# Performance work log

Hardware: AMD Instinct MI355X
Metric: run time of the kernel (lower is better)

## Reference

```python
import jax, jax.numpy as jnp
import numpy as np

EMBED = 768
HEADS = 12
DEPTH = 12
FEAT = 2048


def _ln(x, w, b, eps=1e-6):
    m = x.mean(-1, keepdims=True)
    v = ((x - m) ** 2).mean(-1, keepdims=True)
    return (x - m) * jax.lax.rsqrt(v + eps) * w + b


def _var_attn(x, mbias, Wqkv, bqkv, Wp, bp, h, f):
    # x: (B, N, D) with N = 1 + f*n ; mbias: (B, N) additive mask (0 or -100)
    B, N, D = x.shape
    d = D // h
    n = (N - 1) // f
    scale = d ** -0.5
    qkv = x @ Wqkv.T + bqkv
    q, k, v = jnp.split(qkv, 3, axis=-1)
    hd = lambda t: t.reshape(B, N, h, d).transpose(0, 2, 1, 3)  # (B,h,N,d)
    q = hd(q) * scale
    k = hd(k)
    v = hd(v)
    # cls token attends to everything
    cls_sim = jnp.einsum('bhd,bhjd->bhj', q[:, :, 0], k) + mbias[:, None, :]
    cls_out = jnp.einsum('bhj,bhjd->bhd', jax.nn.softmax(cls_sim, axis=-1), v)[:, :, None, :]
    # spatial tokens attend within their frame plus the cls token
    q_ = q[:, :, 1:].reshape(B, h, f, n, d)
    k_ = jnp.concatenate([jnp.broadcast_to(k[:, :, None, 0:1, :], (B, h, f, 1, d)),
                          k[:, :, 1:].reshape(B, h, f, n, d)], axis=3)
    v_ = jnp.concatenate([jnp.broadcast_to(v[:, :, None, 0:1, :], (B, h, f, 1, d)),
                          v[:, :, 1:].reshape(B, h, f, n, d)], axis=3)
    mcat = jnp.concatenate([jnp.broadcast_to(mbias[:, 0][:, None, None], (B, f, 1)),
                            mbias[:, 1:].reshape(B, f, n)], axis=2)  # (B,f,n+1)
    sim = jnp.einsum('bhfid,bhfjd->bhfij', q_, k_) + mcat[:, None, :, None, :]
    out = jnp.einsum('bhfij,bhfjd->bhfid', jax.nn.softmax(sim, axis=-1), v_)
    out = out.reshape(B, h, f * n, d)
    out = jnp.concatenate([cls_out, out], axis=2).transpose(0, 2, 1, 3).reshape(B, N, D)
    return out @ Wp.T + bp


def setup_inputs() -> dict:
    key = jax.random.key(0)
    ks = jax.random.split(key, 12)
    B, F, L = 256, 4, 20
    std = 0.02
    p = {}
    p['x'] = jax.random.normal(ks[0], (B, F, L, 2054), dtype=jnp.float32)
    p['x_mask'] = jax.random.randint(ks[1], (B, F, L), 0, 2, dtype=jnp.int32)
    p['obj_W'] = (jax.random.normal(ks[2], (EMBED, FEAT)) * std).astype(jnp.float32)
    p['obj_b'] = jnp.zeros((EMBED,), jnp.float32)
    p['pos_W'] = (jax.random.normal(ks[3], (EMBED, 6)) * std).astype(jnp.float32)
    p['pos_b'] = jnp.zeros((EMBED,), jnp.float32)
    p['cls_token'] = (jax.random.normal(ks[4], (1, 1, EMBED)) * std).astype(jnp.float32)
    p['cls_pos'] = (jax.random.normal(ks[5], (1, L + 1, EMBED)) * std).astype(jnp.float32)
    p['temporal_embed'] = jnp.zeros((1, F, EMBED), jnp.float32)
    p['ln1_w'] = jnp.ones((DEPTH, EMBED), jnp.float32)
    p['ln1_b'] = jnp.zeros((DEPTH, EMBED), jnp.float32)
    p['ln2_w'] = jnp.ones((DEPTH, EMBED), jnp.float32)
    p['ln2_b'] = jnp.zeros((DEPTH, EMBED), jnp.float32)
    p['qkv_W'] = (jax.random.normal(ks[6], (DEPTH, 3 * EMBED, EMBED)) * std).astype(jnp.float32)
    p['qkv_b'] = jnp.zeros((DEPTH, 3 * EMBED), jnp.float32)
    p['ap_W'] = (jax.random.normal(ks[7], (DEPTH, EMBED, EMBED)) * std).astype(jnp.float32)
    p['ap_b'] = jnp.zeros((DEPTH, EMBED), jnp.float32)
    p['fc1_W'] = (jax.random.normal(ks[8], (DEPTH, 4 * EMBED, EMBED)) * std).astype(jnp.float32)
    p['fc1_b'] = jnp.zeros((DEPTH, 4 * EMBED), jnp.float32)
    p['fc2_W'] = (jax.random.normal(ks[9], (DEPTH, EMBED, 4 * EMBED)) * std).astype(jnp.float32)
    p['fc2_b'] = jnp.zeros((DEPTH, EMBED), jnp.float32)
    p['proj_W'] = (jax.random.normal(ks[10], (256, EMBED)) * std).astype(jnp.float32)
    return p


def reference(x, x_mask, obj_W, obj_b, pos_W, pos_b, cls_token, cls_pos, temporal_embed,
              ln1_w, ln1_b, ln2_w, ln2_b, qkv_W, qkv_b, ap_W, ap_b,
              fc1_W, fc1_b, fc2_W, fc2_b, proj_W):
    B, F, L, _ = x.shape
    tok = x[..., :FEAT] @ obj_W.T + obj_b + (x[..., FEAT:] @ pos_W.T + pos_b)
    tok = tok.reshape(B, F * L, EMBED)
    m = x_mask.reshape(B, F * L).astype(tok.dtype)
    tok = jnp.concatenate([jnp.broadcast_to(cls_token, (B, 1, EMBED)), tok], axis=1)
    m = jnp.concatenate([jnp.ones((B, 1), tok.dtype), m], axis=1)
    mbias = (m - 1.0) * 100.0  # 0 for valid, -100 for padded
    pos_total = jnp.concatenate([cls_pos[:, 0:1, :], jnp.repeat(temporal_embed, L, axis=1)], axis=1)
    tok = tok + pos_total

    def body(xc, p):
        l1w, l1b, qW, qb, aW, ab, l2w, l2b, f1W, f1b, f2W, f2b = p
        a = _var_attn(_ln(xc, l1w, l1b), mbias, qW, qb, aW, ab, HEADS, F)
        xr = xc + a
        xc = xr + (jax.nn.gelu(_ln(xr, l2w, l2b) @ f1W.T + f1b, approximate=False) @ f2W.T + f2b)
        return xc, None

    tok, _ = jax.lax.scan(body, tok, (ln1_w, ln1_b, qkv_W, qkv_b, ap_W, ap_b,
                                      ln2_w, ln2_b, fc1_W, fc1_b, fc2_W, fc2_b))
    return tok @ proj_W.T, mbias
```

## Files before the change

kernel.cpp:

```cpp
#include <hip/hip_runtime.h>

typedef __bf16 bf16;
typedef __bf16 bf16x8 __attribute__((ext_vector_type(8)));
typedef float f32x4 __attribute__((ext_vector_type(4)));

#define EMBED 768
#define HEADS 12
#define DEPTH 12
#define B_ 256
#define F_ 4
#define L_ 20
#define NTOK 81
#define ROWS (B_ * NTOK)
#define SROWS (B_ * F_ * L_)

#define GLOAD16(g, l)                                                              \
    __builtin_amdgcn_global_load_lds((const __attribute__((address_space(1))) void*)(g), \
                                     (__attribute__((address_space(3))) void*)(l), 16, 0, 0)

__device__ __forceinline__ float fast_gelu(float v) {
    float x = v * 0.70710678118654752f;
    float ax = fabsf(x);
    float t = __fdividef(1.f, fmaf(0.3275911f, ax, 1.f));
    float p = ((((1.061405429f * t - 1.453152027f) * t + 1.421413741f) * t -
                0.284496736f) * t + 0.254829592f) * t;
    float e = __expf(-ax * ax);
    float erfv = copysignf(1.f - p * e, x);
    return 0.5f * v * (1.f + erfv);
}

__global__ __launch_bounds__(256) void repack_kernel(const float* __restrict__ x,
                                                     bf16* __restrict__ xr) {
    int row = blockIdx.x;
    const float* src = x + (size_t)row * 2054;
    bf16* dst = xr + (size_t)row * 2048;
    int t = threadIdx.x;
    int e0 = t * 8;
    bf16 tmp[8];
#pragma unroll
    for (int i = 0; i < 4; ++i) {
        float2 v = *(const float2*)&src[e0 + 2 * i];
        tmp[2 * i] = (bf16)v.x;
        tmp[2 * i + 1] = (bf16)v.y;
    }
    *(uint4*)&dst[e0] = *(const uint4*)tmp;
}

__global__ __launch_bounds__(256) void w2bf_kernel(const float* __restrict__ src,
                                                   bf16* __restrict__ dst) {
    size_t i = ((size_t)blockIdx.x * 256 + threadIdx.x) * 8;
    float4 a = *(const float4*)&src[i];
    float4 b = *(const float4*)&src[i + 4];
    bf16 t[8] = {(bf16)a.x, (bf16)a.y, (bf16)a.z, (bf16)a.w,
                 (bf16)b.x, (bf16)b.y, (bf16)b.z, (bf16)b.w};
    *(uint4*)&dst[i] = *(const uint4*)t;
}

template <int FUSE, bool ROWMAP, typename CT>
__global__ __launch_bounds__(256) void gemm_bb(const bf16* __restrict__ A, int lda,
                                               const bf16* __restrict__ W,
                                               const float* __restrict__ bias,
                                               const bf16* __restrict__ R,
                                               CT* __restrict__ C, int N, int K) {
    __shared__ __align__(16) bf16 As[128 * 64];
    __shared__ __align__(16) bf16 Ws[128 * 64];

    const int tid = threadIdx.x;
    const int lane = tid & 63;
    const int wv = tid >> 6;
    const int wm = (wv & 1) * 64;
    const int wn = (wv >> 1) * 64;
    const int lr = lane & 15;
    const int lq = lane >> 4;

    const int GX = gridDim.x;
    const int nwg = GX * gridDim.y;
    const int flat = blockIdx.y * GX + blockIdx.x;
    const int xcd = flat & 7, pos = flat >> 3;
    const int qc = nwg >> 3, rc = nwg & 7;
    const int wg = (xcd < rc ? xcd * (qc + 1) : rc * (qc + 1) + (xcd - rc) * qc) + pos;
    const int n0 = (wg % GX) * 128;
    const int m0 = (wg / GX) * 128;

    const int srow = lane >> 3;
    const int scol = 8 * ((lane & 7) ^ srow);
    const bf16* aB = A + (size_t)(m0 + srow) * lda + scol;
    const bf16* wB = W + (size_t)(n0 + srow) * K + scol;

    f32x4 acc[4][4];
#pragma unroll
    for (int i = 0; i < 4; ++i)
#pragma unroll
        for (int j = 0; j < 4; ++j) acc[i][j] = (f32x4){0.f, 0.f, 0.f, 0.f};

    const int swz = (lr & 7) << 4;

    for (int k0 = 0; k0 < K; k0 += 64) {
#pragma unroll
        for (int i = 0; i < 4; ++i) {
            const int ch = wv * 4 + i;
            GLOAD16(aB + (size_t)(ch * 8) * lda + k0, &As[ch * 512]);
            GLOAD16(wB + (size_t)(ch * 8) * K + k0, &Ws[ch * 512]);
        }
        __syncthreads();
#pragma unroll
        for (int kk = 0; kk < 2; ++kk) {
            const int co = (((kk << 6) | (lq << 4)) ^ swz) >> 1;
            bf16x8 af[4], bw[4];
#pragma unroll
            for (int t = 0; t < 4; ++t) {
                af[t] = *(const bf16x8*)&As[(wm + t * 16 + lr) * 64 + co];
                bw[t] = *(const bf16x8*)&Ws[(wn + t * 16 + lr) * 64 + co];
            }
#pragma unroll
            for (int mi = 0; mi < 4; ++mi)
#pragma unroll
                for (int ni = 0; ni < 4; ++ni)
                    acc[mi][ni] = __builtin_amdgcn_mfma_f32_16x16x32_bf16(af[mi], bw[ni],
                                                                          acc[mi][ni], 0, 0, 0);
        }
        __syncthreads();
    }

#pragma unroll
    for (int mi = 0; mi < 4; ++mi) {
#pragma unroll
        for (int ni = 0; ni < 4; ++ni) {
            int gcol = n0 + wn + ni * 16 + lr;
            float bv = bias ? bias[gcol] : 0.f;
#pragma unroll
            for (int r = 0; r < 4; ++r) {
                int grow = m0 + wm + mi * 16 + lq * 4 + r;
                float v = acc[mi][ni][r] + bv;
                if (FUSE == 1) v = fast_gelu(v);
                if (FUSE == 2) v += (float)R[(size_t)grow * N + gcol];
                int orow = grow;
                if (ROWMAP) orow = grow + grow / 80 + 1;
                C[(size_t)orow * N + gcol] = (CT)v;
            }
        }
    }
}

template <int FUSE, bool ROWMAP, typename CT>
__global__ __launch_bounds__(256) void gemm_bt(const bf16* __restrict__ A, int lda,
                                               const float* __restrict__ W,
                                               const float* __restrict__ bias,
                                               const bf16* __restrict__ R,
                                               CT* __restrict__ C, int N, int K) {
    __shared__ __align__(16) bf16 As[128][32];
    __shared__ __align__(16) bf16 Ws[128][32];

    const int tid = threadIdx.x;
    const int lane = tid & 63;
    const int wv = tid >> 6;
    const int wm = (wv & 1) * 64;
    const int wn = (wv >> 1) * 64;
    const int lr = lane & 15;
    const int lq = lane >> 4;
    const int m0 = blockIdx.x * 128;
    const int n0 = blockIdx.y * 128;

    f32x4 acc[4][4];
#pragma unroll
    for (int i = 0; i < 4; ++i)
#pragma unroll
        for (int j = 0; j < 4; ++j) acc[i][j] = (f32x4){0.f, 0.f, 0.f, 0.f};

    for (int k0 = 0; k0 < K; k0 += 32) {
#pragma unroll
        for (int i = 0; i < 2; ++i) {
            int c = tid + 256 * i;
            int row = c >> 2;
            int kc = (c & 3) * 8;
            *(uint4*)&As[row][kc] = *(const uint4*)&A[(size_t)(m0 + row) * lda + k0 + kc];
        }
#pragma unroll
        for (int i = 0; i < 4; ++i) {
            int c = tid + 256 * i;
            int row = c >> 3;
            int kc = (c & 7) * 4;
            float4 v = *(const float4*)&W[(size_t)(n0 + row) * K + k0 + kc];
            bf16 wb[4] = {(bf16)v.x, (bf16)v.y, (bf16)v.z, (bf16)v.w};
            *(uint2*)&Ws[row][kc] = *(const uint2*)wb;
        }
        __syncthreads();
        bf16x8 af[4], bf_[4];
#pragma unroll
        for (int t = 0; t < 4; ++t) {
            af[t] = *(const bf16x8*)&As[wm + t * 16 + lr][lq * 8];
            bf_[t] = *(const bf16x8*)&Ws[wn + t * 16 + lr][lq * 8];
        }
#pragma unroll
        for (int mi = 0; mi < 4; ++mi)
#pragma unroll
            for (int ni = 0; ni < 4; ++ni)
                acc[mi][ni] = __builtin_amdgcn_mfma_f32_16x16x32_bf16(af[mi], bf_[ni],
                                                                      acc[mi][ni], 0, 0, 0);
        __syncthreads();
    }

#pragma unroll
    for (int mi = 0; mi < 4; ++mi) {
#pragma unroll
        for (int ni = 0; ni < 4; ++ni) {
            int gcol = n0 + wn + ni * 16 + lr;
            float bv = bias ? bias[gcol] : 0.f;
#pragma unroll
            for (int r = 0; r < 4; ++r) {
                int grow = m0 + wm + mi * 16 + lq * 4 + r;
                float v = acc[mi][ni][r] + bv;
                if (FUSE == 1) v = fast_gelu(v);
                if (FUSE == 2) v += (float)R[(size_t)grow * N + gcol];
                int orow = grow;
                if (ROWMAP) orow = grow + grow / 80 + 1;
                C[(size_t)orow * N + gcol] = (CT)v;
            }
        }
    }
}

__global__ __launch_bounds__(256) void embed_finish(const float* __restrict__ x,
                                                    const float* __restrict__ posW,
                                                    const float* __restrict__ posb,
                                                    const float* __restrict__ temb,
                                                    bf16* __restrict__ tok) {
    int r = blockIdx.x;
    int fr = (r % 80) / 20;
    int orow = r + r / 80 + 1;
    __shared__ float pf[6];
    if (threadIdx.x < 6) pf[threadIdx.x] = x[(size_t)r * 2054 + 2048 + threadIdx.x];
    __syncthreads();
    int t = threadIdx.x;
#pragma unroll
    for (int i = 0; i < 3; ++i) {
        int c = t + 256 * i;
        float v = posb[c] + temb[fr * EMBED + c];
#pragma unroll
        for (int j = 0; j < 6; ++j) v += pf[j] * posW[c * 6 + j];
        size_t idx = (size_t)orow * EMBED + c;
        tok[idx] = (bf16)((float)tok[idx] + v);
    }
}

__global__ __launch_bounds__(256) void cls_mbias_kernel(const float* __restrict__ cls_tok,
                                                        const float* __restrict__ cls_pos,
                                                        const int* __restrict__ xmask,
                                                        bf16* __restrict__ tok,
                                                        float* __restrict__ mbias,
                                                        float* __restrict__ out1) {
    int b = blockIdx.x;
    int t = threadIdx.x;
#pragma unroll
    for (int i = 0; i < 3; ++i) {
        int c = t + 256 * i;
        tok[(size_t)(b * NTOK) * EMBED + c] = (bf16)(cls_tok[c] + cls_pos[c]);
    }
    if (t < NTOK) {
        float mv = (t == 0) ? 0.f : ((float)xmask[b * 80 + t - 1] - 1.f) * 100.f;
        mbias[b * NTOK + t] = mv;
        out1[b * NTOK + t] = mv;
    }
}

__global__ __launch_bounds__(256) void ln_kernel(const bf16* __restrict__ X,
                                                 const float* __restrict__ w,
                                                 const float* __restrict__ b,
                                                 bf16* __restrict__ Y) {
    int row = blockIdx.x;
    int t = threadIdx.x;
    float xv[8];
    float s = 0.f, ss = 0.f;
    if (t < 96) {
        bf16x8 v8 = *(const bf16x8*)&X[(size_t)row * EMBED + t * 8];
#pragma unroll
        for (int i = 0; i < 8; ++i) {
            float v = (float)v8[i];
            xv[i] = v;
            s += v;
            ss += v * v;
        }
    }
#pragma unroll
    for (int off = 32; off; off >>= 1) {
        s += __shfl_down(s, off);
        ss += __shfl_down(ss, off);
    }
    __shared__ float ws_s[4], ws_q[4];
    int wv = t >> 6, lane = t & 63;
    if (lane == 0) { ws_s[wv] = s; ws_q[wv] = ss; }
    __syncthreads();
    s = ws_s[0] + ws_s[1];
    ss = ws_q[0] + ws_q[1];
    float mean = s * (1.f / 768.f);
    float var = ss * (1.f / 768.f) - mean * mean;
    float inv = rsqrtf(fmaxf(var, 0.f) + 1e-6f);
    if (t < 96) {
        float4 w0 = *(const float4*)&w[t * 8];
        float4 w1 = *(const float4*)&w[t * 8 + 4];
        float4 b0 = *(const float4*)&b[t * 8];
        float4 b1 = *(const float4*)&b[t * 8 + 4];
        float wr[8] = {w0.x, w0.y, w0.z, w0.w, w1.x, w1.y, w1.z, w1.w};
        float br[8] = {b0.x, b0.y, b0.z, b0.w, b1.x, b1.y, b1.z, b1.w};
        bf16 ob[8];
#pragma unroll
        for (int i = 0; i < 8; ++i) ob[i] = (bf16)((xv[i] - mean) * inv * wr[i] + br[i]);
        *(uint4*)&Y[(size_t)row * EMBED + t * 8] = *(const uint4*)ob;
    }
}

__global__ __launch_bounds__(256) void attn_kernel(const bf16* __restrict__ qkv,
                                                   const float* __restrict__ mbias,
                                                   bf16* __restrict__ aout) {
    int bh = blockIdx.x;
    int b = bh / HEADS, h = bh % HEADS;
    __shared__ __align__(16) float Qf[NTOK][68];
    __shared__ __align__(16) float Kf[NTOK][68];
    __shared__ __align__(16) bf16 Vs[NTOK][72];
    __shared__ float S[80][22];
    __shared__ float Sc[96];
    __shared__ float MB[NTOK];
    const size_t base = (size_t)(b * NTOK) * 2304 + h * 64;
    int t = threadIdx.x;

    for (int ch = t; ch < NTOK * 8; ch += 256) {
        int r = ch >> 3, c8 = (ch & 7) * 8;
        size_t o = base + (size_t)r * 2304 + c8;
        bf16x8 qv = *(const bf16x8*)&qkv[o];
        bf16x8 kv = *(const bf16x8*)&qkv[o + 768];
        *(uint4*)&Vs[r][c8] = *(const uint4*)&qkv[o + 1536];
        float4 q0 = {(float)qv[0], (float)qv[1], (float)qv[2], (float)qv[3]};
        float4 q1 = {(float)qv[4], (float)qv[5], (float)qv[6], (float)qv[7]};
        float4 k0 = {(float)kv[0], (float)kv[1], (float)kv[2], (float)kv[3]};
        float4 k1 = {(float)kv[4], (float)kv[5], (float)kv[6], (float)kv[7]};
        *(float4*)&Qf[r][c8] = q0;
        *(float4*)&Qf[r][c8 + 4] = q1;
        *(float4*)&Kf[r][c8] = k0;
        *(float4*)&Kf[r][c8 + 4] = k1;
    }
    if (t < NTOK) MB[t] = mbias[b * NTOK + t];
    __syncthreads();

    {
        int qt, kst, kstep, klim;
        if (t < 240) {
            int qi = t / 3;
            qt = 1 + qi;
            kst = t - qi * 3;
            kstep = 3;
            klim = 21;
        } else {
            qt = 0;
            kst = t - 240;
            kstep = 16;
            klim = NTOK;
        }
        float fq[64];
#pragma unroll
        for (int i = 0; i < 16; ++i) {
            float4 v = *(const float4*)&Qf[qt][i * 4];
            fq[4 * i] = v.x; fq[4 * i + 1] = v.y; fq[4 * i + 2] = v.z; fq[4 * i + 3] = v.w;
        }
        if (t < 240) {
            int qi = t / 3, fb = (qi / 20) * 20;
            for (int kj = kst; kj < klim; kj += kstep) {
                int kt = (kj == 0) ? 0 : fb + kj;
                float acc = 0.f;
#pragma unroll
                for (int i = 0; i < 16; ++i) {
                    float4 kv = *(const float4*)&Kf[kt][i * 4];
                    acc += fq[4 * i] * kv.x + fq[4 * i + 1] * kv.y +
                           fq[4 * i + 2] * kv.z + fq[4 * i + 3] * kv.w;
                }
                S[qi][kj] = acc * 0.125f + MB[kt];
            }
        } else {
            for (int kt = kst; kt < klim; kt += kstep) {
                float acc = 0.f;
#pragma unroll
                for (int i = 0; i < 16; ++i) {
                    float4 kv = *(const float4*)&Kf[kt][i * 4];
                    acc += fq[4 * i] * kv.x + fq[4 * i + 1] * kv.y +
                           fq[4 * i + 2] * kv.z + fq[4 * i + 3] * kv.w;
                }
                Sc[kt] = acc * 0.125f + MB[kt];
            }
        }
    }
    __syncthreads();

    if (t < 80) {
        float mx = -1e30f;
        for (int j = 0; j < 21; ++j) mx = fmaxf(mx, S[t][j]);
        float sum = 0.f;
        for (int j = 0; j < 21; ++j) { float e = __expf(S[t][j] - mx); S[t][j] = e; sum += e; }
        float rs = 1.f / sum;
        for (int j = 0; j < 21; ++j) S[t][j] *= rs;
    } else if (t == 80) {
        float mx = -1e30f;
        for (int j = 0; j < NTOK; ++j) mx = fmaxf(mx, Sc[j]);
        float sum = 0.f;
        for (int j = 0; j < NTOK; ++j) { float e = __expf(Sc[j] - mx); Sc[j] = e; sum += e; }
        float rs = 1.f / sum;
        for (int j = 0; j < NTOK; ++j) Sc[j] *= rs;
    }
    __syncthreads();

    for (int idx = t; idx < NTOK * 8; idx += 256) {
        int r = idx >> 3, c8 = (idx & 7) * 8;
        float acc[8];
#pragma unroll
        for (int q = 0; q < 8; ++q) acc[q] = 0.f;
        if (r == 0) {
            for (int j = 0; j < NTOK; ++j) {
                float w = Sc[j];
                bf16x8 vv = *(const bf16x8*)&Vs[j][c8];
#pragma unroll
                for (int q = 0; q < 8; ++q) acc[q] += w * (float)vv[q];
            }
        } else {
            int qi = r - 1, fb = (qi / 20) * 20;
            {
                float w = S[qi][0];
                bf16x8 vv = *(const bf16x8*)&Vs[0][c8];
#pragma unroll
                for (int q = 0; q < 8; ++q) acc[q] += w * (float)vv[q];
            }
            for (int j = 1; j < 21; ++j) {
                float w = S[qi][j];
                bf16x8 vv = *(const bf16x8*)&Vs[fb + j][c8];
#pragma unroll
                for (int q = 0; q < 8; ++q) acc[q] += w * (float)vv[q];
            }
        }
        bf16 ob[8];
#pragma unroll
        for (int q = 0; q < 8; ++q) ob[q] = (bf16)acc[q];
        *(uint4*)&aout[(size_t)(b * NTOK + r) * EMBED + h * 64 + c8] = *(const uint4*)ob;
    }
}

extern "C" void kernel_launch(void* const* d_in, const int* in_sizes, int n_in,
                              void* d_out, int out_size, void* d_ws, size_t ws_size,
                              hipStream_t stream) {
    const float* x = (const float*)d_in[0];
    const int* xmask = (const int*)d_in[1];
    const float* objW = (const float*)d_in[2];
    const float* objb = (const float*)d_in[3];
    const float* posW = (const float*)d_in[4];
    const float* posb = (const float*)d_in[5];
    const float* clsT = (const float*)d_in[6];
    const float* clsP = (const float*)d_in[7];
    const float* temb = (const float*)d_in[8];
    const float* ln1w = (const float*)d_in[9];
    const float* ln1b = (const float*)d_in[10];
    const float* ln2w = (const float*)d_in[11];
    const float* ln2b = (const float*)d_in[12];
    const float* qkvW = (const float*)d_in[13];
    const float* qkvb = (const float*)d_in[14];
    const float* apW = (const float*)d_in[15];
    const float* apb = (const float*)d_in[16];
    const float* f1W = (const float*)d_in[17];
    const float* f1b = (const float*)d_in[18];
    const float* f2W = (const float*)d_in[19];
    const float* f2b = (const float*)d_in[20];
    const float* projW = (const float*)d_in[21];

    char* ws = (char*)d_ws;
    bf16* tok = (bf16*)(ws);
    bf16* s1 = (bf16*)(ws + (size_t)(32 << 20));
    float* mb = (float*)(ws + (size_t)(64 << 20));
    bf16* big = (bf16*)(ws + (size_t)(65 << 20));
    float* out0 = (float*)d_out;
    float* out1 = out0 + (size_t)ROWS * 256;

    const size_t WOFF = (size_t)192 << 20;
    const size_t E_OBJ = (size_t)768 * 2048;
    const size_t E_QKV = (size_t)DEPTH * 2304 * 768;
    const size_t E_AP = (size_t)DEPTH * 768 * 768;
    const size_t E_FC = (size_t)DEPTH * 3072 * 768;
    const size_t E_PROJ = (size_t)256 * 768;
    const size_t WTOT = (E_OBJ + E_QKV + E_AP + 2 * E_FC + E_PROJ) * 2;
    const bool bigws = ws_size >= WOFF + WTOT;

    if (bigws) {
        bf16* objW16 = (bf16*)(ws + WOFF);
        bf16* qkvW16 = objW16 + E_OBJ;
        bf16* apW16 = qkvW16 + E_QKV;
        bf16* fc1W16 = apW16 + E_AP;
        bf16* fc2W16 = fc1W16 + E_FC;
        bf16* projW16 = fc2W16 + E_FC;

        w2bf_kernel<<<(int)(E_OBJ / 2048), 256, 0, stream>>>(objW, objW16);
        w2bf_kernel<<<(int)(E_QKV / 2048), 256, 0, stream>>>(qkvW, qkvW16);
        w2bf_kernel<<<(int)(E_AP / 2048), 256, 0, stream>>>(apW, apW16);
        w2bf_kernel<<<(int)(E_FC / 2048), 256, 0, stream>>>(f1W, fc1W16);
        w2bf_kernel<<<(int)(E_FC / 2048), 256, 0, stream>>>(f2W, fc2W16);
        w2bf_kernel<<<(int)(E_PROJ / 2048), 256, 0, stream>>>(projW, projW16);

        repack_kernel<<<SROWS, 256, 0, stream>>>(x, big);
        gemm_bb<0, true, bf16><<<dim3(EMBED / 128, SROWS / 128), 256, 0, stream>>>(
            big, 2048, objW16, objb, nullptr, tok, EMBED, 2048);
        embed_finish<<<SROWS, 256, 0, stream>>>(x, posW, posb, temb, tok);
        cls_mbias_kernel<<<B_, 256, 0, stream>>>(clsT, clsP, xmask, tok, mb, out1);

        for (int l = 0; l < DEPTH; ++l) {
            ln_kernel<<<ROWS, 256, 0, stream>>>(tok, ln1w + l * EMBED, ln1b + l * EMBED, s1);
            gemm_bb<0, false, bf16><<<dim3(2304 / 128, ROWS / 128), 256, 0, stream>>>(
                s1, EMBED, qkvW16 + (size_t)l * 2304 * 768, qkvb + l * 2304, nullptr, big,
                2304, EMBED);
            attn_kernel<<<B_ * HEADS, 256, 0, stream>>>(big, mb, s1);
            gemm_bb<2, false, bf16><<<dim3(EMBED / 128, ROWS / 128), 256, 0, stream>>>(
                s1, EMBED, apW16 + (size_t)l * 768 * 768, apb + l * EMBED, tok, tok, EMBED,
                EMBED);
            ln_kernel<<<ROWS, 256, 0, stream>>>(tok, ln2w + l * EMBED, ln2b + l * EMBED, s1);
            gemm_bb<1, false, bf16><<<dim3(3072 / 128, ROWS / 128), 256, 0, stream>>>(
                s1, EMBED, fc1W16 + (size_t)l * 3072 * 768, f1b + l * 3072, nullptr, big,
                3072, EMBED);
            gemm_bb<2, false, bf16><<<dim3(EMBED / 128, ROWS / 128), 256, 0, stream>>>(
                big, 3072, fc2W16 + (size_t)l * 3072 * 768, f2b + l * EMBED, tok, tok, EMBED,
                3072);
        }

        gemm_bb<0, false, float><<<dim3(256 / 128, ROWS / 128), 256, 0, stream>>>(
            tok, EMBED, projW16, nullptr, nullptr, out0, 256, EMBED);
    } else {
        repack_kernel<<<SROWS, 256, 0, stream>>>(x, big);
        gemm_bt<0, true, bf16><<<dim3(SROWS / 128, EMBED / 128), 256, 0, stream>>>(
            big, 2048, objW, objb, nullptr, tok, EMBED, 2048);
        embed_finish<<<SROWS, 256, 0, stream>>>(x, posW, posb, temb, tok);
        cls_mbias_kernel<<<B_, 256, 0, stream>>>(clsT, clsP, xmask, tok, mb, out1);

        for (int l = 0; l < DEPTH; ++l) {
            ln_kernel<<<ROWS, 256, 0, stream>>>(tok, ln1w + l * EMBED, ln1b + l * EMBED, s1);
            gemm_bt<0, false, bf16><<<dim3(ROWS / 128, 2304 / 128), 256, 0, stream>>>(
                s1, EMBED, qkvW + (size_t)l * 2304 * EMBED, qkvb + l * 2304, nullptr, big,
                2304, EMBED);
            attn_kernel<<<B_ * HEADS, 256, 0, stream>>>(big, mb, s1);
            gemm_bt<2, false, bf16><<<dim3(ROWS / 128, EMBED / 128), 256, 0, stream>>>(
                s1, EMBED, apW + (size_t)l * EMBED * EMBED, apb + l * EMBED, tok, tok, EMBED,
                EMBED);
            ln_kernel<<<ROWS, 256, 0, stream>>>(tok, ln2w + l * EMBED, ln2b + l * EMBED, s1);
            gemm_bt<1, false, bf16><<<dim3(ROWS / 128, 3072 / 128), 256, 0, stream>>>(
                s1, EMBED, f1W + (size_t)l * 3072 * EMBED, f1b + l * 3072, nullptr, big, 3072,
                EMBED);
            gemm_bt<2, false, bf16><<<dim3(ROWS / 128, EMBED / 128), 256, 0, stream>>>(
                big, 3072, f2W + (size_t)l * EMBED * 3072, f2b + l * EMBED, tok, tok, EMBED,
                3072);
        }

        gemm_bt<0, false, float><<<dim3(ROWS / 128, 256 / 128), 256, 0, stream>>>(
            tok, EMBED, projW, nullptr, nullptr, out0, 256, EMBED);
    }
}
```

Baseline: 7.552 ms.

## Stage GEMM epilogue through LDS for vectorized stores; pack two rows per LN block

The bf16 GEMM epilogue now writes each 16-row accumulator tile into a per-wave LDS patch, then reads it back so each lane handles 8 contiguous columns. This allows 16-byte vector loads of the residual and vector stores of the output, replacing scattered 2-byte accesses. LayerNorm now processes two rows per 256-thread block instead of one, so fewer threads sit idle and half as many blocks are launched. The attention score loop was also cleaned up by simplifying its index setup. The staging adds LDS round trips in the epilogue.

```diff
diff --git a/kernel.cpp b/kernel.cpp
--- a/kernel.cpp
+++ b/kernel.cpp
@@ -62,8 +62,7 @@
                                                const float* __restrict__ bias,
                                                const bf16* __restrict__ R,
                                                CT* __restrict__ C, int N, int K) {
-    __shared__ __align__(16) bf16 As[128 * 64];
-    __shared__ __align__(16) bf16 Ws[128 * 64];
+    __shared__ __align__(16) char smem[32768];
 
     const int tid = threadIdx.x;
     const int lane = tid & 63;
@@ -87,6 +86,9 @@
     const bf16* aB = A + (size_t)(m0 + srow) * lda + scol;
     const bf16* wB = W + (size_t)(n0 + srow) * K + scol;
 
+    bf16* As = (bf16*)smem;
+    bf16* Ws = (bf16*)(smem + 16384);
+
     f32x4 acc[4][4];
 #pragma unroll
     for (int i = 0; i < 4; ++i)
@@ -99,8 +101,8 @@
 #pragma unroll
         for (int i = 0; i < 4; ++i) {
             const int ch = wv * 4 + i;
-            GLOAD16(aB + (size_t)(ch * 8) * lda + k0, &As[ch * 512]);
-            GLOAD16(wB + (size_t)(ch * 8) * K + k0, &Ws[ch * 512]);
+            GLOAD16(aB + (size_t)(ch * 8) * lda + k0, smem + ch * 1024);
+            GLOAD16(wB + (size_t)(ch * 8) * K + k0, smem + 16384 + ch * 1024);
         }
         __syncthreads();
 #pragma unroll
@@ -122,21 +124,46 @@
         __syncthreads();
     }
 
+    float* patch = (float*)(smem + wv * 4352);
+    float bv4[4];
+#pragma unroll
+    for (int ni = 0; ni < 4; ++ni) bv4[ni] = bias ? bias[n0 + wn + ni * 16 + lr] : 0.f;
+    const int rr = lane >> 3;
+    const int c8 = (lane & 7) * 8;
 #pragma unroll
     for (int mi = 0; mi < 4; ++mi) {
 #pragma unroll
-        for (int ni = 0; ni < 4; ++ni) {
-            int gcol = n0 + wn + ni * 16 + lr;
-            float bv = bias ? bias[gcol] : 0.f;
-#pragma unroll
-            for (int r = 0; r < 4; ++r) {
-                int grow = m0 + wm + mi * 16 + lq * 4 + r;
-                float v = acc[mi][ni][r] + bv;
-                if (FUSE == 1) v = fast_gelu(v);
-                if (FUSE == 2) v += (float)R[(size_t)grow * N + gcol];
-                int orow = grow;
-                if (ROWMAP) orow = grow + grow / 80 + 1;
-                C[(size_t)orow * N + gcol] = (CT)v;
+        for (int ni = 0; ni < 4; ++ni)
+#pragma unroll
+            for (int r = 0; r < 4; ++r)
+                patch[(lq * 4 + r) * 68 + ni * 16 + lr] = acc[mi][ni][r] + bv4[ni];
+#pragma unroll
+        for (int hf = 0; hf < 2; ++hf) {
+            int row = rr + hf * 8;
+            float v[8];
+            *(float4*)&v[0] = *(const float4*)&patch[row * 68 + c8];
+            *(float4*)&v[4] = *(const float4*)&patch[row * 68 + c8 + 4];
+            int grow = m0 + wm + mi * 16 + row;
+            int gcol = n0 + wn + c8;
+            if (FUSE == 1) {
+#pragma unroll
+                for (int q = 0; q < 8; ++q) v[q] = fast_gelu(v[q]);
+            }
+            if (FUSE == 2) {
+                bf16x8 rv = *(const bf16x8*)&R[(size_t)grow * N + gcol];
+#pragma unroll
+                for (int q = 0; q < 8; ++q) v[q] += (float)rv[q];
+            }
+            int orow = grow;
+            if (ROWMAP) orow = grow + grow / 80 + 1;
+            if constexpr (sizeof(CT) == 2) {
+                bf16 ob[8];
+#pragma unroll
+                for (int q = 0; q < 8; ++q) ob[q] = (bf16)v[q];
+                *(uint4*)&C[(size_t)orow * N + gcol] = *(const uint4*)ob;
+            } else {
+                *(float4*)&C[(size_t)orow * N + gcol] = *(const float4*)&v[0];
+                *(float4*)&C[(size_t)orow * N + gcol + 4] = *(const float4*)&v[4];
             }
         }
     }
@@ -267,12 +294,13 @@
                                                  const float* __restrict__ w,
                                                  const float* __restrict__ b,
                                                  bf16* __restrict__ Y) {
-    int row = blockIdx.x;
-    int t = threadIdx.x;
+    int half = threadIdx.x >> 7;
+    int row = blockIdx.x * 2 + half;
+    int tt = threadIdx.x & 127;
     float xv[8];
     float s = 0.f, ss = 0.f;
-    if (t < 96) {
-        bf16x8 v8 = *(const bf16x8*)&X[(size_t)row * EMBED + t * 8];
+    if (tt < 96) {
+        bf16x8 v8 = *(const bf16x8*)&X[(size_t)row * EMBED + tt * 8];
 #pragma unroll
         for (int i = 0; i < 8; ++i) {
             float v = (float)v8[i];
@@ -287,25 +315,25 @@
         ss += __shfl_down(ss, off);
     }
     __shared__ float ws_s[4], ws_q[4];
-    int wv = t >> 6, lane = t & 63;
+    int wv = threadIdx.x >> 6, lane = threadIdx.x & 63;
     if (lane == 0) { ws_s[wv] = s; ws_q[wv] = ss; }
     __syncthreads();
-    s = ws_s[0] + ws_s[1];
-    ss = ws_q[0] + ws_q[1];
+    s = ws_s[half * 2] + ws_s[half * 2 + 1];
+    ss = ws_q[half * 2] + ws_q[half * 2 + 1];
     float mean = s * (1.f / 768.f);
     float var = ss * (1.f / 768.f) - mean * mean;
     float inv = rsqrtf(fmaxf(var, 0.f) + 1e-6f);
-    if (t < 96) {
-        float4 w0 = *(const float4*)&w[t * 8];
-        float4 w1 = *(const float4*)&w[t * 8 + 4];
-        float4 b0 = *(const float4*)&b[t * 8];
-        float4 b1 = *(const float4*)&b[t * 8 + 4];
+    if (tt < 96) {
+        float4 w0 = *(const float4*)&w[tt * 8];
+        float4 w1 = *(const float4*)&w[tt * 8 + 4];
+        float4 b0 = *(const float4*)&b[tt * 8];
+        float4 b1 = *(const float4*)&b[tt * 8 + 4];
         float wr[8] = {w0.x, w0.y, w0.z, w0.w, w1.x, w1.y, w1.z, w1.w};
         float br[8] = {b0.x, b0.y, b0.z, b0.w, b1.x, b1.y, b1.z, b1.w};
         bf16 ob[8];
 #pragma unroll
         for (int i = 0; i < 8; ++i) ob[i] = (bf16)((xv[i] - mean) * inv * wr[i] + br[i]);
-        *(uint4*)&Y[(size_t)row * EMBED + t * 8] = *(const uint4*)ob;
+        *(uint4*)&Y[(size_t)row * EMBED + tt * 8] = *(const uint4*)ob;
     }
 }
 
@@ -342,18 +370,11 @@
     __syncthreads();
 
     {
-        int qt, kst, kstep, klim;
+        int qt;
         if (t < 240) {
-            int qi = t / 3;
-            qt = 1 + qi;
-            kst = t - qi * 3;
-            kstep = 3;
-            klim = 21;
+            qt = 1 + t / 3;
         } else {
             qt = 0;
-            kst = t - 240;
-            kstep = 16;
-            klim = NTOK;
         }
         float fq[64];
 #pragma unroll
@@ -362,8 +383,8 @@
             fq[4 * i] = v.x; fq[4 * i + 1] = v.y; fq[4 * i + 2] = v.z; fq[4 * i + 3] = v.w;
         }
         if (t < 240) {
-            int qi = t / 3, fb = (qi / 20) * 20;
-            for (int kj = kst; kj < klim; kj += kstep) {
+            int qi = t / 3, fb = (qi / 20) * 20, kst = t - qi * 3;
+            for (int kj = kst; kj < 21; kj += 3) {
                 int kt = (kj == 0) ? 0 : fb + kj;
                 float acc = 0.f;
 #pragma unroll
@@ -375,7 +396,7 @@
                 S[qi][kj] = acc * 0.125f + MB[kt];
             }
         } else {
-            for (int kt = kst; kt < klim; kt += kstep) {
+            for (int kt = t - 240; kt < NTOK; kt += 16) {
                 float acc = 0.f;
 #pragma unroll
                 for (int i = 0; i < 16; ++i) {
@@ -505,7 +526,7 @@
         cls_mbias_kernel<<<B_, 256, 0, stream>>>(clsT, clsP, xmask, tok, mb, out1);
 
         for (int l = 0; l < DEPTH; ++l) {
-            ln_kernel<<<ROWS, 256, 0, stream>>>(tok, ln1w + l * EMBED, ln1b + l * EMBED, s1);
+            ln_kernel<<<ROWS / 2, 256, 0, stream>>>(tok, ln1w + l * EMBED, ln1b + l * EMBED, s1);
             gemm_bb<0, false, bf16><<<dim3(2304 / 128, ROWS / 128), 256, 0, stream>>>(
                 s1, EMBED, qkvW16 + (size_t)l * 2304 * 768, qkvb + l * 2304, nullptr, big,
                 2304, EMBED);
@@ -513,7 +534,7 @@
             gemm_bb<2, false, bf16><<<dim3(EMBED / 128, ROWS / 128), 256, 0, stream>>>(
                 s1, EMBED, apW16 + (size_t)l * 768 * 768, apb + l * EMBED, tok, tok, EMBED,
                 EMBED);
-            ln_kernel<<<ROWS, 256, 0, stream>>>(tok, ln2w + l * EMBED, ln2b + l * EMBED, s1);
+            ln_kernel<<<ROWS / 2, 256, 0, stream>>>(tok, ln2w + l * EMBED, ln2b + l * EMBED, s1);
             gemm_bb<1, false, bf16><<<dim3(3072 / 128, ROWS / 128), 256, 0, stream>>>(
                 s1, EMBED, fc1W16 + (size_t)l * 3072 * 768, f1b + l * 3072, nullptr, big,
                 3072, EMBED);
@@ -532,7 +553,7 @@
         cls_mbias_kernel<<<B_, 256, 0, stream>>>(clsT, clsP, xmask, tok, mb, out1);
 
         for (int l = 0; l < DEPTH; ++l) {
-            ln_kernel<<<ROWS, 256, 0, stream>>>(tok, ln1w + l * EMBED, ln1b + l * EMBED, s1);
+            ln_kernel<<<ROWS / 2, 256, 0, stream>>>(tok, ln1w + l * EMBED, ln1b + l * EMBED, s1);
             gemm_bt<0, false, bf16><<<dim3(ROWS / 128, 2304 / 128), 256, 0, stream>>>(
                 s1, EMBED, qkvW + (size_t)l * 2304 * EMBED, qkvb + l * 2304, nullptr, big,
                 2304, EMBED);
@@ -540,7 +561,7 @@
             gemm_bt<2, false, bf16><<<dim3(ROWS / 128, EMBED / 128), 256, 0, stream>>>(
                 s1, EMBED, apW + (size_t)l * EMBED * EMBED, apb + l * EMBED, tok, tok, EMBED,
                 EMBED);
-            ln_kernel<<<ROWS, 256, 0, stream>>>(tok, ln2w + l * EMBED, ln2b + l * EMBED, s1);
+            ln_kernel<<<ROWS / 2, 256, 0, stream>>>(tok, ln2w + l * EMBED, ln2b + l * EMBED, s1);
             gemm_bt<1, false, bf16><<<dim3(ROWS / 128, 3072 / 128), 256, 0, stream>>>(
                 s1, EMBED, f1W + (size_t)l * 3072 * EMBED, f1b + l * 3072, nullptr, big, 3072,
                 EMBED);
```

Result: no change. 7.406 ms (-1.9%).
